# Optimization experiments

Measured on AMD Instinct MI355X. Metric: run time of the kernel, lower is better.

The kernel has to match this reference:

```python
import jax, jax.numpy as jnp
import numpy as np

B = 32768; NF = 8; E = 16; V = 100000; D = 4
IN = 2 * NF * E          # 256 = id_dims + agn_dims
FCN = [256, 128, 64]
DIMS = [IN] + FCN
EPS = 1e-5               # BatchNorm1d eps


def setup_inputs() -> dict:
    ks = jax.random.split(jax.random.key(0), 64)
    inp = {
        'id_idx': jax.random.randint(ks[0], (B, NF), 0, V),
        'agn_idx': jax.random.randint(ks[1], (B, NF), 0, V),
        'domain_id': jax.random.randint(ks[2], (B,), 0, D),
        'id_tables': jax.random.normal(ks[3], (NF, V, E), dtype=jnp.float32) * 0.01,
        'agn_tables': jax.random.normal(ks[4], (NF, V, E), dtype=jnp.float32) * 0.01,
    }
    k = 5
    for i in range(len(FCN)):
        din, dout = DIMS[i], DIMS[i + 1]
        inp[f'mlp_W{i}'] = jax.random.normal(ks[k], (D, din, dout), dtype=jnp.float32) / np.sqrt(din).astype(np.float32); k += 1
        inp[f'mlp_b{i}'] = jnp.zeros((D, dout), jnp.float32)
        inp[f'bn_g{i}'] = jnp.ones((D, dout), jnp.float32)
        inp[f'bn_b{i}'] = jnp.zeros((D, dout), jnp.float32)
        inp[f'gate_W1_{i}'] = jax.random.normal(ks[k], (D, IN, dout), dtype=jnp.float32) / np.sqrt(IN).astype(np.float32); k += 1
        inp[f'gate_b1_{i}'] = jnp.zeros((D, dout), jnp.float32)
        inp[f'gate_W2_{i}'] = jax.random.normal(ks[k], (D, dout, dout), dtype=jnp.float32) / np.sqrt(dout).astype(np.float32); k += 1
        inp[f'gate_b2_{i}'] = jnp.zeros((D, dout), jnp.float32)
    inp['fin_W'] = jax.random.normal(ks[k], (D, DIMS[-1], 1), dtype=jnp.float32) / np.sqrt(DIMS[-1]).astype(np.float32)
    inp['fin_b'] = jnp.zeros((D, 1), jnp.float32)
    return inp


def _embed(tables, idx):
    # tables [NF,V,E], idx [B,NF] -> [B, NF*E] (per-feature lookup then concat)
    g = tables[jnp.arange(NF)[None, :], idx]            # [B,NF,E]
    return g.reshape(idx.shape[0], NF * E)


def _ppnet(id_tables, agn_tables, mlp_W, mlp_b, bn_g, bn_b, gW1, gb1, gW2, gb2,
           fin_W, fin_b, id_idx, agn_idx, domain_id):
    id_x = _embed(id_tables, id_idx)                    # [B, 128]
    agn_x = _embed(agn_tables, agn_idx)                 # [B, 128]
    # gate_input = cat(id_x, agn_x.detach())
    gate_in = jnp.concatenate([id_x, jax.lax.stop_gradient(agn_x)], axis=1)  # [B, IN]
    h = None
    for i in range(len(FCN)):
        # GateNU: Linear->ReLU->Linear->2*sigmoid, broadcast over D domain towers
        g1 = jax.nn.relu(jnp.einsum('bi,dio->dbo', gate_in, gW1[i]) + gb1[i][:, None, :])
        gate = 2.0 * jax.nn.sigmoid(jnp.einsum('dbo,dop->dbp', g1, gW2[i]) + gb2[i][:, None, :])
        # MLP layer: Linear -> BatchNorm1d (train-mode batch stats) -> ReLU
        if h is None:
            h = jnp.einsum('bi,dio->dbo', gate_in, mlp_W[i]) + mlp_b[i][:, None, :]
        else:
            h = jnp.einsum('dbi,dio->dbo', h, mlp_W[i]) + mlp_b[i][:, None, :]
        mu = h.mean(axis=1, keepdims=True)
        var = h.var(axis=1, keepdims=True)              # biased, matches torch BN training
        h = (h - mu) * jax.lax.rsqrt(var + EPS) * bn_g[i][:, None, :] + bn_b[i][:, None, :]
        h = jax.nn.relu(h)
        h = h * gate
    out = jax.nn.sigmoid(jnp.einsum('dbh,dho->dbo', h, fin_W) + fin_b[:, None, :])  # [D,B,1]
    out = out[:, :, 0]                                  # [D,B]
    # torch.where masked-select chain == gather the row of the assigned domain
    return out[domain_id, jnp.arange(out.shape[1])]     # [B]


def reference(id_idx, agn_idx, domain_id, id_tables, agn_tables,
              mlp_W0, mlp_b0, bn_g0, bn_b0, gate_W1_0, gate_b1_0, gate_W2_0, gate_b2_0,
              mlp_W1, mlp_b1, bn_g1, bn_b1, gate_W1_1, gate_b1_1, gate_W2_1, gate_b2_1,
              mlp_W2, mlp_b2, bn_g2, bn_b2, gate_W1_2, gate_b1_2, gate_W2_2, gate_b2_2,
              fin_W, fin_b):
    mlp_W = [mlp_W0, mlp_W1, mlp_W2]; mlp_b = [mlp_b0, mlp_b1, mlp_b2]
    bn_g = [bn_g0, bn_g1, bn_g2]; bn_b = [bn_b0, bn_b1, bn_b2]
    gW1 = [gate_W1_0, gate_W1_1, gate_W1_2]; gb1 = [gate_b1_0, gate_b1_1, gate_b1_2]
    gW2 = [gate_W2_0, gate_W2_1, gate_W2_2]; gb2 = [gate_b2_0, gate_b2_1, gate_b2_2]
    return _ppnet(id_tables, agn_tables, mlp_W, mlp_b, bn_g, bn_b, gW1, gb1, gW2, gb2,
                  fin_W, fin_b, id_idx, agn_idx, domain_id)
```

## Files before the change

### kernel.cpp

```cpp
#include <hip/hip_runtime.h>


typedef __attribute__((ext_vector_type(8))) short short8;
typedef __attribute__((ext_vector_type(4))) float floatx4;

#define BATCH 32768
#define NDOM 4
#define TM 64

__device__ __forceinline__ unsigned short f2b(float f) {
    unsigned u = __float_as_uint(f);
    u += 0x7fffu + ((u >> 16) & 1u);
    return (unsigned short)(u >> 16);
}
__device__ __forceinline__ float b2f(unsigned short h) {
    return __uint_as_float(((unsigned)h) << 16);
}

struct MatDesc { const float* src; unsigned K, N, pfx, total; };
struct PrepArgs { MatDesc m[9]; float* stats; unsigned statsN; unsigned grand; };

__global__ __launch_bounds__(256) void prep_k(PrepArgs a, unsigned short* __restrict__ wt) {
    unsigned e = blockIdx.x * 256 + threadIdx.x;
    if (e < a.statsN) a.stats[e] = 0.f;
    if (e >= a.grand) return;
    int j = 0;
    while (j < 8 && e >= a.m[j].pfx + a.m[j].total) j++;
    const unsigned K = a.m[j].K, N = a.m[j].N;
    const unsigned local = e - a.m[j].pfx;
    const unsigned kn = K * N;
    const unsigned d = local / kn;
    const unsigned r2 = local - d * kn;
    const unsigned n = r2 / K;
    const unsigned k = r2 - n * K;
    wt[e] = f2b(a.m[j].src[((long long)d * K + k) * N + n]);
}

__global__ __launch_bounds__(256) void embed_k(const int* __restrict__ idi, const int* __restrict__ agi,
                                               const float* __restrict__ idt, const float* __restrict__ agt,
                                               unsigned short* __restrict__ gin) {
    int t = blockIdx.x * 256 + threadIdx.x;
    int b = t >> 4, slot = t & 15;
    int f = slot & 7;
    const int* ip = (slot < 8) ? idi : agi;
    const float* tab = (slot < 8) ? idt : agt;
    int ix = ip[b * 8 + f];
    const float* src = tab + ((long long)f * 100000 + ix) * 16;
    unsigned short tmp[16];
#pragma unroll
    for (int j = 0; j < 16; j++) tmp[j] = f2b(src[j]);
    unsigned short* dst = gin + (long long)b * 256 + slot * 16;
    *(uint4*)dst = *(const uint4*)tmp;
    *(uint4*)(dst + 8) = *(const uint4*)(tmp + 8);
}

__global__ __launch_bounds__(256, 2) void stats_k(
    const unsigned short* __restrict__ X,
    const unsigned short* __restrict__ Wm,
    float* __restrict__ gsum, float* __restrict__ gssq) {
    constexpr int N = 256, KX = 256, GX = KX / 8, CT = 4;
    __shared__ __align__(16) unsigned short tA[TM * KX];
    const int t = threadIdx.x;
    const int d = blockIdx.y;
    const int m0 = blockIdx.x * TM;
    const unsigned short* Xp = X + (long long)m0 * KX;
#pragma unroll
    for (int r = 0; r < TM * GX / 256; r++) {
        int idx = r * 256 + t;
        int m = idx / GX, j = idx % GX;
        uint4 v = *(const uint4*)(Xp + (long long)m * KX + j * 8);
        *(uint4*)&tA[(m * GX + (j ^ (m & 7))) * 8] = v;
    }
    __syncthreads();
    const int w = t >> 6, lane = t & 63, lrow = lane & 15, lq = lane >> 4;
    const int n0w = w * 64;
    const unsigned short* Wp = Wm + ((long long)d * N + n0w) * KX;
    floatx4 acc[4][CT];
#pragma unroll
    for (int rt = 0; rt < 4; rt++)
#pragma unroll
        for (int ct = 0; ct < CT; ct++) acc[rt][ct] = (floatx4)(0.f);
#pragma unroll
    for (int k0 = 0; k0 < KX; k0 += 32) {
        short8 a[4], b[CT];
#pragma unroll
        for (int rt = 0; rt < 4; rt++) {
            int m = rt * 16 + lrow;
            a[rt] = *(const short8*)&tA[(m * GX + (((k0 >> 3) | lq) ^ (m & 7))) * 8];
        }
#pragma unroll
        for (int ct = 0; ct < CT; ct++)
            b[ct] = *(const short8*)(Wp + (long long)(ct * 16 + lrow) * KX + k0 + lq * 8);
#pragma unroll
        for (int rt = 0; rt < 4; rt++)
#pragma unroll
            for (int ct = 0; ct < CT; ct++)
                acc[rt][ct] = __builtin_amdgcn_mfma_f32_16x16x32_bf16(a[rt], b[ct], acc[rt][ct], 0, 0, 0);
    }
#pragma unroll
    for (int ct = 0; ct < CT; ct++) {
        float s = 0.f, ss = 0.f;
#pragma unroll
        for (int rt = 0; rt < 4; rt++)
#pragma unroll
            for (int r = 0; r < 4; r++) { float v = acc[rt][ct][r]; s += v; ss += v * v; }
        s += __shfl_down(s, 32); ss += __shfl_down(ss, 32);
        s += __shfl_down(s, 16); ss += __shfl_down(ss, 16);
        if (lane < 16) {
            atomicAdd(&gsum[d * N + n0w + ct * 16 + lane], s);
            atomicAdd(&gssq[d * N + n0w + ct * 16 + lane], ss);
        }
    }
}

template <int N, int KX, int NN, bool GINH, bool FINAL>
__global__ __launch_bounds__(256, 2) void fused_k(
    const unsigned short* __restrict__ gin,
    const unsigned short* __restrict__ Xh,
    const unsigned short* __restrict__ W1,
    const unsigned short* __restrict__ W2,
    const unsigned short* __restrict__ Wm,
    const unsigned short* __restrict__ WmN,
    const float* __restrict__ gb1, const float* __restrict__ gb2,
    const float* __restrict__ gsum, const float* __restrict__ gssq,
    const float* __restrict__ gma, const float* __restrict__ bta,
    float* __restrict__ gsumN, float* __restrict__ gssqN,
    unsigned short* __restrict__ Xn,
    const int* __restrict__ dom, const float* __restrict__ fw,
    const float* __restrict__ fb, float* __restrict__ outp, float invB) {
    constexpr int GGn = N / 8;
    constexpr int GX = KX / 8;
    constexpr int CT = N / 64;
    constexpr int CTn = (NN > 0) ? (NN / 64) : 1;
    __shared__ __align__(16) unsigned short buf[TM * 256];
    __shared__ float sSC[N], sSH[N];
    __shared__ float sSum[NN > 0 ? NN : 1], sSsq[NN > 0 ? NN : 1];

    const int t = threadIdx.x;
    const int d = blockIdx.y;
    const int m0 = blockIdx.x * TM;
    const int w = t >> 6, lane = t & 63, lrow = lane & 15, lq = lane >> 4;
    const int n0w = w * (N / 4);

    if (t < N) {
        float ma = gsum[d * N + t] * invB;
        float var = gssq[d * N + t] * invB - ma * ma;
        float sc = rsqrtf(var + 1e-5f) * gma[d * N + t];
        sSC[t] = sc;
        sSH[t] = bta[d * N + t] - ma * sc;
    }
    if (NN > 0 && t < NN) { sSum[t] = 0.f; sSsq[t] = 0.f; }

    {
        const unsigned short* Gp = gin + (long long)m0 * 256;
#pragma unroll
        for (int r = 0; r < 8; r++) {
            int idx = r * 256 + t;
            int m = idx >> 5, j = idx & 31;
            uint4 v = *(const uint4*)(Gp + (long long)m * 256 + j * 8);
            *(uint4*)&buf[((m << 5) + (j ^ (m & 7))) * 8] = v;
        }
    }
    __syncthreads();

    floatx4 acc1[4][CT];
#pragma unroll
    for (int rt = 0; rt < 4; rt++)
#pragma unroll
        for (int ct = 0; ct < CT; ct++) acc1[rt][ct] = (floatx4)(0.f);
    {
        const unsigned short* W1p = W1 + ((long long)d * N + n0w) * 256;
#pragma unroll
        for (int k0 = 0; k0 < 256; k0 += 32) {
            short8 a[4], b[CT];
#pragma unroll
            for (int rt = 0; rt < 4; rt++) {
                int m = rt * 16 + lrow;
                a[rt] = *(const short8*)&buf[((m << 5) + (((k0 >> 3) | lq) ^ (m & 7))) * 8];
            }
#pragma unroll
            for (int ct = 0; ct < CT; ct++)
                b[ct] = *(const short8*)(W1p + (long long)(ct * 16 + lrow) * 256 + k0 + lq * 8);
#pragma unroll
            for (int rt = 0; rt < 4; rt++)
#pragma unroll
                for (int ct = 0; ct < CT; ct++)
                    acc1[rt][ct] = __builtin_amdgcn_mfma_f32_16x16x32_bf16(a[rt], b[ct], acc1[rt][ct], 0, 0, 0);
        }
    }
    __syncthreads();
#pragma unroll
    for (int ct = 0; ct < CT; ct++) {
        int n = n0w + ct * 16 + lrow;
        float bs = gb1[d * N + n];
        int jj = n >> 3, sub = n & 7;
#pragma unroll
        for (int rt = 0; rt < 4; rt++)
#pragma unroll
            for (int r = 0; r < 4; r++) {
                int m = rt * 16 + lq * 4 + r;
                buf[(m * GGn + (jj ^ (m & 7))) * 8 + sub] = f2b(fmaxf(acc1[rt][ct][r] + bs, 0.f));
            }
    }
    __syncthreads();

    floatx4 acc2[4][CT];
#pragma unroll
    for (int rt = 0; rt < 4; rt++)
#pragma unroll
        for (int ct = 0; ct < CT; ct++) acc2[rt][ct] = (floatx4)(0.f);
    {
        const unsigned short* W2p = W2 + ((long long)d * N + n0w) * N;
#pragma unroll
        for (int k0 = 0; k0 < N; k0 += 32) {
            short8 a[4], b[CT];
#pragma unroll
            for (int rt = 0; rt < 4; rt++) {
                int m = rt * 16 + lrow;
                a[rt] = *(const short8*)&buf[(m * GGn + ((((k0 >> 3) | lq)) ^ (m & 7))) * 8];
            }
#pragma unroll
            for (int ct = 0; ct < CT; ct++)
                b[ct] = *(const short8*)(W2p + (long long)(ct * 16 + lrow) * N + k0 + lq * 8);
#pragma unroll
            for (int rt = 0; rt < 4; rt++)
#pragma unroll
                for (int ct = 0; ct < CT; ct++)
                    acc2[rt][ct] = __builtin_amdgcn_mfma_f32_16x16x32_bf16(a[rt], b[ct], acc2[rt][ct], 0, 0, 0);
        }
    }
    unsigned gatep[4][CT][2];
#pragma unroll
    for (int ct = 0; ct < CT; ct++) {
        int n = n0w + ct * 16 + lrow;
        float bs = gb2[d * N + n];
#pragma unroll
        for (int rt = 0; rt < 4; rt++) {
            float g0 = 2.f / (1.f + __expf(-(acc2[rt][ct][0] + bs)));
            float g1 = 2.f / (1.f + __expf(-(acc2[rt][ct][1] + bs)));
            float g2 = 2.f / (1.f + __expf(-(acc2[rt][ct][2] + bs)));
            float g3 = 2.f / (1.f + __expf(-(acc2[rt][ct][3] + bs)));
            gatep[rt][ct][0] = (unsigned)f2b(g0) | ((unsigned)f2b(g1) << 16);
            gatep[rt][ct][1] = (unsigned)f2b(g2) | ((unsigned)f2b(g3) << 16);
        }
    }
    __syncthreads();

    {
        const unsigned short* Xp = Xh + ((long long)(GINH ? 0 : d * BATCH) + m0) * KX;
#pragma unroll
        for (int r = 0; r < TM * GX / 256; r++) {
            int idx = r * 256 + t;
            int m = idx / GX, j = idx % GX;
            uint4 v = *(const uint4*)(Xp + (long long)m * KX + j * 8);
            *(uint4*)&buf[(m * GX + (j ^ (m & 7))) * 8] = v;
        }
    }
    __syncthreads();

    floatx4 acch[4][CT];
#pragma unroll
    for (int rt = 0; rt < 4; rt++)
#pragma unroll
        for (int ct = 0; ct < CT; ct++) acch[rt][ct] = (floatx4)(0.f);
    {
        const unsigned short* Wmp = Wm + ((long long)d * N + n0w) * KX;
#pragma unroll
        for (int k0 = 0; k0 < KX; k0 += 32) {
            short8 a[4], b[CT];
#pragma unroll
            for (int rt = 0; rt < 4; rt++) {
                int m = rt * 16 + lrow;
                a[rt] = *(const short8*)&buf[(m * GX + (((k0 >> 3) | lq) ^ (m & 7))) * 8];
            }
#pragma unroll
            for (int ct = 0; ct < CT; ct++)
                b[ct] = *(const short8*)(Wmp + (long long)(ct * 16 + lrow) * KX + k0 + lq * 8);
#pragma unroll
            for (int rt = 0; rt < 4; rt++)
#pragma unroll
                for (int ct = 0; ct < CT; ct++)
                    acch[rt][ct] = __builtin_amdgcn_mfma_f32_16x16x32_bf16(a[rt], b[ct], acch[rt][ct], 0, 0, 0);
        }
    }
    __syncthreads();

#pragma unroll
    for (int ct = 0; ct < CT; ct++) {
        int n = n0w + ct * 16 + lrow;
        float sc = sSC[n], sh = sSH[n];
        int jj = n >> 3, sub = n & 7;
#pragma unroll
        for (int rt = 0; rt < 4; rt++) {
            float gv[4] = {b2f((unsigned short)(gatep[rt][ct][0] & 0xffff)),
                           b2f((unsigned short)(gatep[rt][ct][0] >> 16)),
                           b2f((unsigned short)(gatep[rt][ct][1] & 0xffff)),
                           b2f((unsigned short)(gatep[rt][ct][1] >> 16))};
#pragma unroll
            for (int r = 0; r < 4; r++) {
                int m = rt * 16 + lq * 4 + r;
                float v = fmaxf(acch[rt][ct][r] * sc + sh, 0.f) * gv[r];
                buf[(m * GGn + (jj ^ (m & 7))) * 8 + sub] = f2b(v);
            }
        }
    }
    __syncthreads();

    if (!FINAL) {
        unsigned short* Op = Xn + ((long long)d * BATCH + m0) * N;
#pragma unroll
        for (int r = 0; r < TM * GGn / 256; r++) {
            int idx = r * 256 + t;
            int m = idx / GGn, j = idx % GGn;
            *(uint4*)(Op + (long long)m * N + j * 8) = *(const uint4*)&buf[(m * GGn + (j ^ (m & 7))) * 8];
        }
    } else {
        int m = t >> 2, q = t & 3;
        const float* fwp = fw + d * 64;
        float s = 0.f;
#pragma unroll
        for (int k = 0; k < 16; k++) {
            int c = q * 16 + k;
            s += b2f(buf[(m * 8 + ((c >> 3) ^ (m & 7))) * 8 + (c & 7)]) * fwp[c];
        }
        s += __shfl_down(s, 1);
        s += __shfl_down(s, 2);
        if (q == 0) {
            int b = m0 + m;
            if (dom[b] == d) outp[b] = 1.f / (1.f + __expf(-(s + fb[d])));
        }
    }

    if (NN > 0) {
        const int n0wN = w * (NN / 4);
        floatx4 accs[4][CTn];
#pragma unroll
        for (int rt = 0; rt < 4; rt++)
#pragma unroll
            for (int ct = 0; ct < CTn; ct++) accs[rt][ct] = (floatx4)(0.f);
        const unsigned short* Wnp = WmN + ((long long)d * NN + n0wN) * N;
#pragma unroll
        for (int k0 = 0; k0 < N; k0 += 32) {
            short8 a[4], b[CTn];
#pragma unroll
            for (int rt = 0; rt < 4; rt++) {
                int m = rt * 16 + lrow;
                a[rt] = *(const short8*)&buf[(m * GGn + (((k0 >> 3) | lq) ^ (m & 7))) * 8];
            }
#pragma unroll
            for (int ct = 0; ct < CTn; ct++)
                b[ct] = *(const short8*)(Wnp + (long long)(ct * 16 + lrow) * N + k0 + lq * 8);
#pragma unroll
            for (int rt = 0; rt < 4; rt++)
#pragma unroll
                for (int ct = 0; ct < CTn; ct++)
                    accs[rt][ct] = __builtin_amdgcn_mfma_f32_16x16x32_bf16(a[rt], b[ct], accs[rt][ct], 0, 0, 0);
        }
#pragma unroll
        for (int ct = 0; ct < CTn; ct++) {
            float s = 0.f, ss = 0.f;
#pragma unroll
            for (int rt = 0; rt < 4; rt++)
#pragma unroll
                for (int r = 0; r < 4; r++) { float v = accs[rt][ct][r]; s += v; ss += v * v; }
            s += __shfl_down(s, 32); ss += __shfl_down(ss, 32);
            s += __shfl_down(s, 16); ss += __shfl_down(ss, 16);
            if (lane < 16) {
                atomicAdd(&sSum[n0wN + ct * 16 + lane], s);
                atomicAdd(&sSsq[n0wN + ct * 16 + lane], ss);
            }
        }
        __syncthreads();
        if (t < NN) {
            atomicAdd(&gsumN[d * NN + t], sSum[t]);
            atomicAdd(&gssqN[d * NN + t], sSsq[t]);
        }
    }
}

extern "C" void kernel_launch(void* const* d_in, const int* in_sizes, int n_in,
                              void* d_out, int out_size, void* d_ws, size_t ws_size,
                              hipStream_t stream) {
    const int B = BATCH, D = NDOM;

    const int* id_idx = (const int*)d_in[0];
    const int* agn_idx = (const int*)d_in[1];
    const int* dom = (const int*)d_in[2];
    const float* id_t = (const float*)d_in[3];
    const float* agn_t = (const float*)d_in[4];
    const float *mlpW[3], *bng[3], *bnb[3], *gW1[3], *gb1[3], *gW2[3], *gb2[3];
    for (int i = 0; i < 3; i++) {
        int b0 = 5 + i * 8;
        mlpW[i] = (const float*)d_in[b0 + 0];
        bng[i] = (const float*)d_in[b0 + 2];
        bnb[i] = (const float*)d_in[b0 + 3];
        gW1[i] = (const float*)d_in[b0 + 4];
        gb1[i] = (const float*)d_in[b0 + 5];
        gW2[i] = (const float*)d_in[b0 + 6];
        gb2[i] = (const float*)d_in[b0 + 7];
    }
    const float* finW = (const float*)d_in[29];
    const float* finb = (const float*)d_in[30];

    char* wsc = (char*)d_ws;
    size_t off = 0;
    auto alloc = [&](size_t bytes) -> char* {
        char* p = wsc + off;
        off = (off + bytes + 255) & ~(size_t)255;
        return p;
    };

    struct { const float* src; int K, N; } mats[9] = {
        {mlpW[0], 256, 256}, {gW1[0], 256, 256}, {gW2[0], 256, 256},
        {mlpW[1], 256, 128}, {gW1[1], 256, 128}, {gW2[1], 128, 128},
        {mlpW[2], 128, 64},  {gW1[2], 256, 64},  {gW2[2], 64, 64}};
    unsigned pfx[10];
    pfx[0] = 0;
    for (int j = 0; j < 9; j++) pfx[j + 1] = pfx[j] + 4u * mats[j].K * mats[j].N;

    unsigned short* wt = (unsigned short*)alloc((size_t)pfx[9] * 2);
    unsigned short* gin = (unsigned short*)alloc((size_t)B * 256 * 2);
    float* stats = (float*)alloc((size_t)3 * 2 * D * 256 * 4);
    unsigned short* X1 = (unsigned short*)alloc((size_t)D * B * 256 * 2);
    unsigned short* X2 = (unsigned short*)alloc((size_t)D * B * 128 * 2);

    PrepArgs pa;
    for (int j = 0; j < 9; j++) {
        pa.m[j].src = mats[j].src;
        pa.m[j].K = (unsigned)mats[j].K;
        pa.m[j].N = (unsigned)mats[j].N;
        pa.m[j].pfx = pfx[j];
        pa.m[j].total = 4u * mats[j].K * mats[j].N;
    }
    pa.stats = stats;
    pa.statsN = 3 * 2 * D * 256;
    pa.grand = pfx[9];

    const float invB = 1.f / (float)B;
    dim3 gs(B / TM, D);

    prep_k<<<dim3((pfx[9] + 255) / 256), 256, 0, stream>>>(pa, wt);
    embed_k<<<dim3(B * 16 / 256), 256, 0, stream>>>(id_idx, agn_idx, id_t, agn_t, gin);

    float* gsum0 = stats + 0 * 2 * D * 256; float* gssq0 = gsum0 + D * 256;
    float* gsum1 = stats + 1 * 2 * D * 256; float* gssq1 = gsum1 + D * 256;
    float* gsum2 = stats + 2 * 2 * D * 256; float* gssq2 = gsum2 + D * 256;

    stats_k<<<gs, 256, 0, stream>>>(gin, wt + pfx[0], gsum0, gssq0);

    fused_k<256, 256, 128, true, false><<<gs, 256, 0, stream>>>(
        gin, gin, wt + pfx[1], wt + pfx[2], wt + pfx[0], wt + pfx[3],
        gb1[0], gb2[0], gsum0, gssq0, bng[0], bnb[0], gsum1, gssq1,
        X1, nullptr, nullptr, nullptr, nullptr, invB);

    fused_k<128, 256, 64, false, false><<<gs, 256, 0, stream>>>(
        gin, X1, wt + pfx[4], wt + pfx[5], wt + pfx[3], wt + pfx[6],
        gb1[1], gb2[1], gsum1, gssq1, bng[1], bnb[1], gsum2, gssq2,
        X2, nullptr, nullptr, nullptr, nullptr, invB);

    fused_k<64, 128, 0, false, true><<<gs, 256, 0, stream>>>(
        gin, X2, wt + pfx[7], wt + pfx[8], wt + pfx[6], nullptr,
        gb1[2], gb2[2], gsum2, gssq2, bng[2], bnb[2], nullptr, nullptr,
        nullptr, dom, finW, finb, (float*)d_out, invB);
}
```

Baseline: 527.3 us.

## Fuse embedding gather with layer-0 BN stats and switch LDS to padded layout

Merges the embedding gather kernel and the layer-0 batch-norm statistics GEMM into one kernel. Each block gathers its 64 rows into shared memory, writes them to global memory, and loops over all four domains. This avoids re-reading the gathered input from global memory and drops one launch. Shared-memory tiles across all kernels switch from an XOR-swizzled layout to a row-padded layout (stride K+8). Occupancy hints move from launch_bounds min-blocks to amdgpu_waves_per_eu, which trades grid parallelism in the stats pass (fewer blocks, serial domain loop) and may change register allocation.

```diff
diff --git a/kernel.cpp b/kernel.cpp
--- a/kernel.cpp
+++ b/kernel.cpp
@@ -36,85 +36,92 @@
     wt[e] = f2b(a.m[j].src[((long long)d * K + k) * N + n]);
 }
 
-__global__ __launch_bounds__(256) void embed_k(const int* __restrict__ idi, const int* __restrict__ agi,
-                                               const float* __restrict__ idt, const float* __restrict__ agt,
-                                               unsigned short* __restrict__ gin) {
-    int t = blockIdx.x * 256 + threadIdx.x;
-    int b = t >> 4, slot = t & 15;
-    int f = slot & 7;
-    const int* ip = (slot < 8) ? idi : agi;
-    const float* tab = (slot < 8) ? idt : agt;
-    int ix = ip[b * 8 + f];
-    const float* src = tab + ((long long)f * 100000 + ix) * 16;
-    unsigned short tmp[16];
-#pragma unroll
-    for (int j = 0; j < 16; j++) tmp[j] = f2b(src[j]);
-    unsigned short* dst = gin + (long long)b * 256 + slot * 16;
-    *(uint4*)dst = *(const uint4*)tmp;
-    *(uint4*)(dst + 8) = *(const uint4*)(tmp + 8);
-}
-
-__global__ __launch_bounds__(256, 2) void stats_k(
-    const unsigned short* __restrict__ X,
-    const unsigned short* __restrict__ Wm,
-    float* __restrict__ gsum, float* __restrict__ gssq) {
-    constexpr int N = 256, KX = 256, GX = KX / 8, CT = 4;
-    __shared__ __align__(16) unsigned short tA[TM * KX];
+__global__ __launch_bounds__(256) __attribute__((amdgpu_waves_per_eu(4, 4)))
+void embed_stats_k(const int* __restrict__ idi, const int* __restrict__ agi,
+                   const float* __restrict__ idt, const float* __restrict__ agt,
+                   const unsigned short* __restrict__ Wm0,
+                   unsigned short* __restrict__ gin,
+                   float* __restrict__ gsum, float* __restrict__ gssq) {
+    constexpr int LDP = 264;
+    __shared__ __align__(16) unsigned short buf[TM * LDP];
     const int t = threadIdx.x;
-    const int d = blockIdx.y;
     const int m0 = blockIdx.x * TM;
-    const unsigned short* Xp = X + (long long)m0 * KX;
-#pragma unroll
-    for (int r = 0; r < TM * GX / 256; r++) {
-        int idx = r * 256 + t;
-        int m = idx / GX, j = idx % GX;
-        uint4 v = *(const uint4*)(Xp + (long long)m * KX + j * 8);
-        *(uint4*)&tA[(m * GX + (j ^ (m & 7))) * 8] = v;
-    }
-    __syncthreads();
+
+    {
+        int r = t >> 2, sp = t & 3;
+        int b = m0 + r;
+#pragma unroll
+        for (int ss = 0; ss < 4; ss++) {
+            int s = sp * 4 + ss;
+            int f = s & 7;
+            const int* ip = (s < 8) ? idi : agi;
+            const float* tab = (s < 8) ? idt : agt;
+            int ix = ip[b * 8 + f];
+            const float* src = tab + ((long long)f * 100000 + ix) * 16;
+            unsigned short tmp[16];
+#pragma unroll
+            for (int j = 0; j < 16; j++) tmp[j] = f2b(src[j]);
+            unsigned short* dst = &buf[r * LDP + s * 16];
+            *(uint4*)dst = *(const uint4*)tmp;
+            *(uint4*)(dst + 8) = *(const uint4*)(tmp + 8);
+        }
+    }
+    __syncthreads();
+
+    {
+        unsigned short* Gp = gin + (long long)m0 * 256;
+#pragma unroll
+        for (int it = 0; it < 8; it++) {
+            int idx = it * 256 + t;
+            int m = idx >> 5, j = idx & 31;
+            *(uint4*)(Gp + (long long)m * 256 + j * 8) = *(const uint4*)&buf[m * LDP + j * 8];
+        }
+    }
+
     const int w = t >> 6, lane = t & 63, lrow = lane & 15, lq = lane >> 4;
     const int n0w = w * 64;
-    const unsigned short* Wp = Wm + ((long long)d * N + n0w) * KX;
-    floatx4 acc[4][CT];
-#pragma unroll
-    for (int rt = 0; rt < 4; rt++)
-#pragma unroll
-        for (int ct = 0; ct < CT; ct++) acc[rt][ct] = (floatx4)(0.f);
-#pragma unroll
-    for (int k0 = 0; k0 < KX; k0 += 32) {
-        short8 a[4], b[CT];
-#pragma unroll
-        for (int rt = 0; rt < 4; rt++) {
-            int m = rt * 16 + lrow;
-            a[rt] = *(const short8*)&tA[(m * GX + (((k0 >> 3) | lq) ^ (m & 7))) * 8];
-        }
-#pragma unroll
-        for (int ct = 0; ct < CT; ct++)
-            b[ct] = *(const short8*)(Wp + (long long)(ct * 16 + lrow) * KX + k0 + lq * 8);
+    for (int d = 0; d < NDOM; d++) {
+        const unsigned short* Wp = Wm0 + ((long long)d * 256 + n0w) * 256;
+        floatx4 acc[4][4];
 #pragma unroll
         for (int rt = 0; rt < 4; rt++)
 #pragma unroll
-            for (int ct = 0; ct < CT; ct++)
-                acc[rt][ct] = __builtin_amdgcn_mfma_f32_16x16x32_bf16(a[rt], b[ct], acc[rt][ct], 0, 0, 0);
-    }
-#pragma unroll
-    for (int ct = 0; ct < CT; ct++) {
-        float s = 0.f, ss = 0.f;
-#pragma unroll
-        for (int rt = 0; rt < 4; rt++)
-#pragma unroll
-            for (int r = 0; r < 4; r++) { float v = acc[rt][ct][r]; s += v; ss += v * v; }
-        s += __shfl_down(s, 32); ss += __shfl_down(ss, 32);
-        s += __shfl_down(s, 16); ss += __shfl_down(ss, 16);
-        if (lane < 16) {
-            atomicAdd(&gsum[d * N + n0w + ct * 16 + lane], s);
-            atomicAdd(&gssq[d * N + n0w + ct * 16 + lane], ss);
+            for (int ct = 0; ct < 4; ct++) acc[rt][ct] = (floatx4)(0.f);
+#pragma unroll
+        for (int k0 = 0; k0 < 256; k0 += 32) {
+            short8 a[4], bb[4];
+#pragma unroll
+            for (int rt = 0; rt < 4; rt++)
+                a[rt] = *(const short8*)&buf[(rt * 16 + lrow) * LDP + k0 + lq * 8];
+#pragma unroll
+            for (int ct = 0; ct < 4; ct++)
+                bb[ct] = *(const short8*)(Wp + (long long)(ct * 16 + lrow) * 256 + k0 + lq * 8);
+#pragma unroll
+            for (int rt = 0; rt < 4; rt++)
+#pragma unroll
+                for (int ct = 0; ct < 4; ct++)
+                    acc[rt][ct] = __builtin_amdgcn_mfma_f32_16x16x32_bf16(a[rt], bb[ct], acc[rt][ct], 0, 0, 0);
+        }
+#pragma unroll
+        for (int ct = 0; ct < 4; ct++) {
+            float s = 0.f, ss = 0.f;
+#pragma unroll
+            for (int rt = 0; rt < 4; rt++)
+#pragma unroll
+                for (int r = 0; r < 4; r++) { float v = acc[rt][ct][r]; s += v; ss += v * v; }
+            s += __shfl_down(s, 32); ss += __shfl_down(ss, 32);
+            s += __shfl_down(s, 16); ss += __shfl_down(ss, 16);
+            if (lane < 16) {
+                atomicAdd(&gsum[d * 256 + n0w + ct * 16 + lane], s);
+                atomicAdd(&gssq[d * 256 + n0w + ct * 16 + lane], ss);
+            }
         }
     }
 }
 
 template <int N, int KX, int NN, bool GINH, bool FINAL>
-__global__ __launch_bounds__(256, 2) void fused_k(
+__global__ __launch_bounds__(256) __attribute__((amdgpu_waves_per_eu(3, 3)))
+void fused_k(
     const unsigned short* __restrict__ gin,
     const unsigned short* __restrict__ Xh,
     const unsigned short* __restrict__ W1,
@@ -128,11 +135,12 @@
     unsigned short* __restrict__ Xn,
     const int* __restrict__ dom, const float* __restrict__ fw,
     const float* __restrict__ fb, float* __restrict__ outp, float invB) {
-    constexpr int GGn = N / 8;
-    constexpr int GX = KX / 8;
+    constexpr int LDG = 264;
+    constexpr int LDN = N + 8;
+    constexpr int LDX = KX + 8;
     constexpr int CT = N / 64;
     constexpr int CTn = (NN > 0) ? (NN / 64) : 1;
-    __shared__ __align__(16) unsigned short buf[TM * 256];
+    __shared__ __align__(16) unsigned short buf[TM * LDG];
     __shared__ float sSC[N], sSH[N];
     __shared__ float sSum[NN > 0 ? NN : 1], sSsq[NN > 0 ? NN : 1];
 
@@ -154,11 +162,10 @@
     {
         const unsigned short* Gp = gin + (long long)m0 * 256;
 #pragma unroll
-        for (int r = 0; r < 8; r++) {
-            int idx = r * 256 + t;
+        for (int it = 0; it < 8; it++) {
+            int idx = it * 256 + t;
             int m = idx >> 5, j = idx & 31;
-            uint4 v = *(const uint4*)(Gp + (long long)m * 256 + j * 8);
-            *(uint4*)&buf[((m << 5) + (j ^ (m & 7))) * 8] = v;
+            *(uint4*)&buf[m * LDG + j * 8] = *(const uint4*)(Gp + (long long)m * 256 + j * 8);
         }
     }
     __syncthreads();
@@ -174,10 +181,8 @@
         for (int k0 = 0; k0 < 256; k0 += 32) {
             short8 a[4], b[CT];
 #pragma unroll
-            for (int rt = 0; rt < 4; rt++) {
-                int m = rt * 16 + lrow;
-                a[rt] = *(const short8*)&buf[((m << 5) + (((k0 >> 3) | lq) ^ (m & 7))) * 8];
-            }
+            for (int rt = 0; rt < 4; rt++)
+                a[rt] = *(const short8*)&buf[(rt * 16 + lrow) * LDG + k0 + lq * 8];
 #pragma unroll
             for (int ct = 0; ct < CT; ct++)
                 b[ct] = *(const short8*)(W1p + (long long)(ct * 16 + lrow) * 256 + k0 + lq * 8);
@@ -193,13 +198,12 @@
     for (int ct = 0; ct < CT; ct++) {
         int n = n0w + ct * 16 + lrow;
         float bs = gb1[d * N + n];
-        int jj = n >> 3, sub = n & 7;
 #pragma unroll
         for (int rt = 0; rt < 4; rt++)
 #pragma unroll
             for (int r = 0; r < 4; r++) {
                 int m = rt * 16 + lq * 4 + r;
-                buf[(m * GGn + (jj ^ (m & 7))) * 8 + sub] = f2b(fmaxf(acc1[rt][ct][r] + bs, 0.f));
+                buf[m * LDN + n] = f2b(fmaxf(acc1[rt][ct][r] + bs, 0.f));
             }
     }
     __syncthreads();
@@ -215,10 +219,8 @@
         for (int k0 = 0; k0 < N; k0 += 32) {
             short8 a[4], b[CT];
 #pragma unroll
-            for (int rt = 0; rt < 4; rt++) {
-                int m = rt * 16 + lrow;
-                a[rt] = *(const short8*)&buf[(m * GGn + ((((k0 >> 3) | lq)) ^ (m & 7))) * 8];
-            }
+            for (int rt = 0; rt < 4; rt++)
+                a[rt] = *(const short8*)&buf[(rt * 16 + lrow) * LDN + k0 + lq * 8];
 #pragma unroll
             for (int ct = 0; ct < CT; ct++)
                 b[ct] = *(const short8*)(W2p + (long long)(ct * 16 + lrow) * N + k0 + lq * 8);
@@ -247,13 +249,13 @@
     __syncthreads();
 
     {
-        const unsigned short* Xp = Xh + ((long long)(GINH ? 0 : d * BATCH) + m0) * KX;
-#pragma unroll
-        for (int r = 0; r < TM * GX / 256; r++) {
-            int idx = r * 256 + t;
-            int m = idx / GX, j = idx % GX;
-            uint4 v = *(const uint4*)(Xp + (long long)m * KX + j * 8);
-            *(uint4*)&buf[(m * GX + (j ^ (m & 7))) * 8] = v;
+        const unsigned short* Xp = GINH ? (gin + (long long)m0 * KX)
+                                        : (Xh + ((long long)d * BATCH + m0) * KX);
+#pragma unroll
+        for (int it = 0; it < KX / 32; it++) {
+            int idx = it * 256 + t;
+            int m = idx / (KX / 8), j = idx % (KX / 8);
+            *(uint4*)&buf[m * LDX + j * 8] = *(const uint4*)(Xp + (long long)m * KX + j * 8);
         }
     }
     __syncthreads();
@@ -269,10 +271,8 @@
         for (int k0 = 0; k0 < KX; k0 += 32) {
             short8 a[4], b[CT];
 #pragma unroll
-            for (int rt = 0; rt < 4; rt++) {
-                int m = rt * 16 + lrow;
-                a[rt] = *(const short8*)&buf[(m * GX + (((k0 >> 3) | lq) ^ (m & 7))) * 8];
-            }
+            for (int rt = 0; rt < 4; rt++)
+                a[rt] = *(const short8*)&buf[(rt * 16 + lrow) * LDX + k0 + lq * 8];
 #pragma unroll
             for (int ct = 0; ct < CT; ct++)
                 b[ct] = *(const short8*)(Wmp + (long long)(ct * 16 + lrow) * KX + k0 + lq * 8);
@@ -289,7 +289,6 @@
     for (int ct = 0; ct < CT; ct++) {
         int n = n0w + ct * 16 + lrow;
         float sc = sSC[n], sh = sSH[n];
-        int jj = n >> 3, sub = n & 7;
 #pragma unroll
         for (int rt = 0; rt < 4; rt++) {
             float gv[4] = {b2f((unsigned short)(gatep[rt][ct][0] & 0xffff)),
@@ -300,7 +299,7 @@
             for (int r = 0; r < 4; r++) {
                 int m = rt * 16 + lq * 4 + r;
                 float v = fmaxf(acch[rt][ct][r] * sc + sh, 0.f) * gv[r];
-                buf[(m * GGn + (jj ^ (m & 7))) * 8 + sub] = f2b(v);
+                buf[m * LDN + n] = f2b(v);
             }
         }
     }
@@ -309,10 +308,10 @@
     if (!FINAL) {
         unsigned short* Op = Xn + ((long long)d * BATCH + m0) * N;
 #pragma unroll
-        for (int r = 0; r < TM * GGn / 256; r++) {
-            int idx = r * 256 + t;
-            int m = idx / GGn, j = idx % GGn;
-            *(uint4*)(Op + (long long)m * N + j * 8) = *(const uint4*)&buf[(m * GGn + (j ^ (m & 7))) * 8];
+        for (int it = 0; it < TM * (N / 8) / 256; it++) {
+            int idx = it * 256 + t;
+            int m = idx / (N / 8), j = idx % (N / 8);
+            *(uint4*)(Op + (long long)m * N + j * 8) = *(const uint4*)&buf[m * LDN + j * 8];
         }
     } else {
         int m = t >> 2, q = t & 3;
@@ -321,7 +320,7 @@
 #pragma unroll
         for (int k = 0; k < 16; k++) {
             int c = q * 16 + k;
-            s += b2f(buf[(m * 8 + ((c >> 3) ^ (m & 7))) * 8 + (c & 7)]) * fwp[c];
+            s += b2f(buf[m * LDN + c]) * fwp[c];
         }
         s += __shfl_down(s, 1);
         s += __shfl_down(s, 2);
@@ -343,10 +342,8 @@
         for (int k0 = 0; k0 < N; k0 += 32) {
             short8 a[4], b[CTn];
 #pragma unroll
-            for (int rt = 0; rt < 4; rt++) {
-                int m = rt * 16 + lrow;
-                a[rt] = *(const short8*)&buf[(m * GGn + (((k0 >> 3) | lq) ^ (m & 7))) * 8];
-            }
+            for (int rt = 0; rt < 4; rt++)
+                a[rt] = *(const short8*)&buf[(rt * 16 + lrow) * LDN + k0 + lq * 8];
 #pragma unroll
             for (int ct = 0; ct < CTn; ct++)
                 b[ct] = *(const short8*)(Wnp + (long long)(ct * 16 + lrow) * N + k0 + lq * 8);
@@ -439,14 +436,14 @@
     const float invB = 1.f / (float)B;
     dim3 gs(B / TM, D);
 
-    prep_k<<<dim3((pfx[9] + 255) / 256), 256, 0, stream>>>(pa, wt);
-    embed_k<<<dim3(B * 16 / 256), 256, 0, stream>>>(id_idx, agn_idx, id_t, agn_t, gin);
-
     float* gsum0 = stats + 0 * 2 * D * 256; float* gssq0 = gsum0 + D * 256;
     float* gsum1 = stats + 1 * 2 * D * 256; float* gssq1 = gsum1 + D * 256;
     float* gsum2 = stats + 2 * 2 * D * 256; float* gssq2 = gsum2 + D * 256;
 
-    stats_k<<<gs, 256, 0, stream>>>(gin, wt + pfx[0], gsum0, gssq0);
+    prep_k<<<dim3((pfx[9] + 255) / 256), 256, 0, stream>>>(pa, wt);
+
+    embed_stats_k<<<dim3(B / TM), 256, 0, stream>>>(id_idx, agn_idx, id_t, agn_t,
+                                                    wt + pfx[0], gin, gsum0, gssq0);
 
     fused_k<256, 256, 128, true, false><<<gs, 256, 0, stream>>>(
         gin, gin, wt + pfx[1], wt + pfx[2], wt + pfx[0], wt + pfx[3],
```

After: 550.0 us. 1.04x slower.
